# Kernel tuning notes

Measured on AMD Instinct MI355X. Metric: run time of the kernel, lower is better.

Reference implementation:

```python
import jax, jax.numpy as jnp
import numpy as np

NUM_HEADS = 32
NUM_KV_HEADS = 8
HEAD_DIM = 128
EPS = 1e-6
ROPE_THETA = 10000.0


def setup_inputs() -> dict:
    key = jax.random.key(0)
    k1, k2, k3 = jax.random.split(key, 3)
    B, S, H = 2, 2048, 4096
    qkv_out = (NUM_HEADS + 2 * NUM_KV_HEADS) * HEAD_DIM  # 6144
    return {
        "hidden_states": jax.random.normal(k1, (B, S, H), dtype=jnp.float32),
        "positions": jnp.arange(S, dtype=jnp.int32),
        "wqkv": jax.random.normal(k2, (qkv_out, H), dtype=jnp.float32) * 0.02,
        "q_norm_w": jnp.ones((HEAD_DIM,), dtype=jnp.float32),
        "k_norm_w": jnp.ones((HEAD_DIM,), dtype=jnp.float32),
        "wo": jax.random.normal(k3, (H, H), dtype=jnp.float32) * 0.02,
    }


def _rmsnorm(x, w, eps=EPS):
    # per-head RMSNorm over last dim (head_dim), computed in fp32
    xf = x.astype(jnp.float32)
    var = jnp.mean(xf * xf, axis=-1, keepdims=True)
    return (xf * jax.lax.rsqrt(var + eps) * w).astype(x.dtype)


def _rope(x, positions):
    # NeoX-style half rotation, rotary_dim == head_dim
    d = x.shape[-1]
    half = d // 2
    inv_freq = 1.0 / (ROPE_THETA ** (jnp.arange(0, half, dtype=jnp.float32) * 2.0 / d))
    ang = positions.astype(jnp.float32)[:, None] * inv_freq[None, :]  # [S, half]
    cos = jnp.cos(ang)[None, :, None, :]  # [1,S,1,half]
    sin = jnp.sin(ang)[None, :, None, :]
    x1, x2 = x[..., :half], x[..., half:]
    return jnp.concatenate([x1 * cos - x2 * sin, x2 * cos + x1 * sin], axis=-1)


def reference(hidden_states, positions, wqkv, q_norm_w, k_norm_w, wo):
    B, S, H = hidden_states.shape
    scale = HEAD_DIM ** -0.5
    qkv = jnp.einsum("bsh,oh->bso", hidden_states, wqkv)
    q_size = NUM_HEADS * HEAD_DIM
    kv_size = NUM_KV_HEADS * HEAD_DIM
    q = qkv[..., :q_size].reshape(B, S, NUM_HEADS, HEAD_DIM)
    k = qkv[..., q_size:q_size + kv_size].reshape(B, S, NUM_KV_HEADS, HEAD_DIM)
    v = qkv[..., q_size + kv_size:].reshape(B, S, NUM_KV_HEADS, HEAD_DIM)
    q = _rmsnorm(q, q_norm_w)
    k = _rmsnorm(k, k_norm_w)
    q = _rope(q, positions)
    k = _rope(k, positions)
    # GQA: expand kv heads to query heads
    group = NUM_HEADS // NUM_KV_HEADS
    k = jnp.repeat(k, group, axis=2)  # [B,S,NUM_HEADS,D]
    v = jnp.repeat(v, group, axis=2)
    scores = jnp.einsum("bqhd,bkhd->bhqk", q, k) * scale
    causal = jnp.tril(jnp.ones((S, S), dtype=bool))
    scores = jnp.where(causal[None, None], scores, jnp.finfo(scores.dtype).min)
    probs = jax.nn.softmax(scores, axis=-1)
    attn = jnp.einsum("bhqk,bkhd->bqhd", probs, v).reshape(B, S, NUM_HEADS * HEAD_DIM)
    return jnp.einsum("bsi,oi->bso", attn, wo)
```

## Files before the change

### kernel.cpp

```cpp
#include <hip/hip_runtime.h>
#include <hip/hip_bf16.h>
#include <cstdint>
#include <cstddef>

typedef __hip_bfloat16 bf16;
typedef __attribute__((ext_vector_type(8))) short s8v;
typedef __attribute__((ext_vector_type(4))) float f4v;

#define NH 32
#define NKV 8
#define HD 128
#define BB 2
#define SS 2048
#define HH 4096
#define QKVO 6144
#define MM 4096

__device__ __forceinline__ void gld_lds16(const void* g, void* l) {
    __builtin_amdgcn_global_load_lds(
        (const __attribute__((address_space(1))) void*)g,
        (__attribute__((address_space(3))) void*)l, 16, 0, 0);
}

#define MFMA_BF16(a, b, c) __builtin_amdgcn_mfma_f32_16x16x32_bf16((a), (b), (c), 0, 0, 0)

struct alignas(16) bf16x8s { bf16 v[8]; };
__global__ __launch_bounds__(256) void conv_kernel(const float* __restrict__ in,
                                                   bf16* __restrict__ out, int n8) {
    int i = blockIdx.x * 256 + threadIdx.x;
    if (i >= n8) return;
    const float4* in4 = (const float4*)in;
    float4 a = in4[i * 2];
    float4 b = in4[i * 2 + 1];
    bf16x8s p;
    p.v[0] = __float2bfloat16(a.x); p.v[1] = __float2bfloat16(a.y);
    p.v[2] = __float2bfloat16(a.z); p.v[3] = __float2bfloat16(a.w);
    p.v[4] = __float2bfloat16(b.x); p.v[5] = __float2bfloat16(b.y);
    p.v[6] = __float2bfloat16(b.z); p.v[7] = __float2bfloat16(b.w);
    *(bf16x8s*)(out + (size_t)i * 8) = p;
}

__device__ __forceinline__ void stage_half(const bf16* __restrict__ gbase, int ldg,
                                           int kt, int h, bf16* lbase, int tid) {
    int srow = tid >> 3;
    int slot = (tid & 7) ^ (srow & 7);
    const bf16* g = gbase + (size_t)(h * 128 + srow) * ldg + (size_t)kt * 64 + slot * 8;
    char* l = (char*)lbase + h * 16384 + tid * 16;
    gld_lds16(g, l);
    gld_lds16(g + (size_t)64 * ldg, l + 8192);
}

template <typename OutT>
__global__ __launch_bounds__(512, 2) void gemm_bt256(const bf16* __restrict__ A,
                                                     const bf16* __restrict__ Bm,
                                                     OutT* __restrict__ C,
                                                     int M, int N, int K) {
    __shared__ bf16 sA[2][256 * 64];
    __shared__ bf16 sB[2][256 * 64];
    const int tid = threadIdx.x;
    const int lane = tid & 63;
    const int wave = tid >> 6;
    const int l15 = lane & 15, quad = lane >> 4;
    const int wm = wave >> 2;
    const int wn = wave & 3;

    const int nbn = N >> 8;
    const int nwg = (M >> 8) * nbn;
    const int orig = blockIdx.y * gridDim.x + blockIdx.x;
    const int cpx = nwg >> 3;
    const int swz = (orig & 7) * cpx + (orig >> 3);
    const int bm = swz / nbn, bn = swz % nbn;

    const bf16* Ab = A + (size_t)bm * 256 * K;
    const bf16* Bb = Bm + (size_t)bn * 256 * K;
    const int NT = K >> 6;

    const int soff0 = (quad ^ (l15 & 7)) << 4;
    const int ra  = (wm * 128 + l15) * 128;
    const int rbb = (wn * 64 + l15) * 128;
#define LDA(p, m, k) (*(const s8v*)((const char*)sA[p] + ra  + (m) * 2048 + (soff0 ^ ((k) << 6))))
#define LDB(p, n, k) (*(const s8v*)((const char*)sB[p] + rbb + (n) * 2048 + (soff0 ^ ((k) << 6))))

    f4v acc[8][4] = {};
    s8v a[4][2], b0[2][2], b1[2][2];

    stage_half(Bb, K, 0, 0, sB[0], tid);
    stage_half(Ab, K, 0, 0, sA[0], tid);
    stage_half(Bb, K, 0, 1, sB[0], tid);
    stage_half(Ab, K, 0, 1, sA[0], tid);
    stage_half(Bb, K, 1, 0, sB[1], tid);
    stage_half(Ab, K, 1, 0, sA[1], tid);
    asm volatile("s_waitcnt vmcnt(4)" ::: "memory");
    __builtin_amdgcn_s_barrier();

    for (int t = 0; t < NT; ++t) {
        const int p = t & 1;
#pragma unroll
        for (int m = 0; m < 4; ++m) { a[m][0] = LDA(p, m, 0); a[m][1] = LDA(p, m, 1); }
#pragma unroll
        for (int n = 0; n < 2; ++n) { b0[n][0] = LDB(p, n, 0); b0[n][1] = LDB(p, n, 1); }
        if (t + 1 < NT) stage_half(Bb, K, t + 1, 1, sB[p ^ 1], tid);
        asm volatile("s_waitcnt lgkmcnt(8)" ::: "memory");
        __builtin_amdgcn_s_barrier();
        asm volatile("s_waitcnt lgkmcnt(0)" ::: "memory");
        __builtin_amdgcn_sched_barrier(0);
        __builtin_amdgcn_s_setprio(1);
#pragma unroll
        for (int m = 0; m < 4; ++m)
#pragma unroll
            for (int n = 0; n < 2; ++n) {
                acc[m][n] = MFMA_BF16(a[m][0], b0[n][0], acc[m][n]);
                acc[m][n] = MFMA_BF16(a[m][1], b0[n][1], acc[m][n]);
            }
        __builtin_amdgcn_s_setprio(0);
        __builtin_amdgcn_s_barrier();
#pragma unroll
        for (int n = 0; n < 2; ++n) { b1[n][0] = LDB(p, n + 2, 0); b1[n][1] = LDB(p, n + 2, 1); }
        if (t + 1 < NT) stage_half(Ab, K, t + 1, 1, sA[p ^ 1], tid);
        __builtin_amdgcn_s_barrier();
        asm volatile("s_waitcnt lgkmcnt(0)" ::: "memory");
        __builtin_amdgcn_sched_barrier(0);
        __builtin_amdgcn_s_setprio(1);
#pragma unroll
        for (int m = 0; m < 4; ++m)
#pragma unroll
            for (int n = 0; n < 2; ++n) {
                acc[m][n + 2] = MFMA_BF16(a[m][0], b1[n][0], acc[m][n + 2]);
                acc[m][n + 2] = MFMA_BF16(a[m][1], b1[n][1], acc[m][n + 2]);
            }
        __builtin_amdgcn_s_setprio(0);
        __builtin_amdgcn_s_barrier();
#pragma unroll
        for (int m = 0; m < 4; ++m) { a[m][0] = LDA(p, m + 4, 0); a[m][1] = LDA(p, m + 4, 1); }
        if (t + 2 < NT) stage_half(Bb, K, t + 2, 0, sB[p], tid);
        __builtin_amdgcn_s_barrier();
        asm volatile("s_waitcnt lgkmcnt(0)" ::: "memory");
        __builtin_amdgcn_sched_barrier(0);
        __builtin_amdgcn_s_setprio(1);
#pragma unroll
        for (int m = 0; m < 4; ++m)
#pragma unroll
            for (int n = 0; n < 2; ++n) {
                acc[m + 4][n + 2] = MFMA_BF16(a[m][0], b1[n][0], acc[m + 4][n + 2]);
                acc[m + 4][n + 2] = MFMA_BF16(a[m][1], b1[n][1], acc[m + 4][n + 2]);
            }
        __builtin_amdgcn_s_setprio(0);
        __builtin_amdgcn_s_barrier();
        if (t + 2 < NT) stage_half(Ab, K, t + 2, 0, sA[p], tid);
        __builtin_amdgcn_s_barrier();
        __builtin_amdgcn_s_setprio(1);
#pragma unroll
        for (int m = 0; m < 4; ++m)
#pragma unroll
            for (int n = 0; n < 2; ++n) {
                acc[m + 4][n] = MFMA_BF16(a[m][0], b0[n][0], acc[m + 4][n]);
                acc[m + 4][n] = MFMA_BF16(a[m][1], b0[n][1], acc[m + 4][n]);
            }
        __builtin_amdgcn_s_setprio(0);
        if (t + 2 < NT) { asm volatile("s_waitcnt vmcnt(4)" ::: "memory"); }
        else            { asm volatile("s_waitcnt vmcnt(0)" ::: "memory"); }
        __builtin_amdgcn_s_barrier();
    }
#undef LDA
#undef LDB

#pragma unroll
    for (int m = 0; m < 8; ++m)
#pragma unroll
        for (int n = 0; n < 4; ++n) {
            int r0 = bm * 256 + wm * 128 + m * 16 + quad * 4;
            int c0 = bn * 256 + wn * 64 + n * 16 + l15;
#pragma unroll
            for (int r = 0; r < 4; ++r) {
                float v = acc[m][n][r];
                if constexpr (sizeof(OutT) == 2)
                    C[(size_t)(r0 + r) * N + c0] = (OutT)__float2bfloat16(v);
                else
                    C[(size_t)(r0 + r) * N + c0] = (OutT)v;
            }
        }
}

__global__ __launch_bounds__(128) void norm_rope_kernel(
    const bf16* __restrict__ qkv, const int* __restrict__ positions,
    const float* __restrict__ qw, const float* __restrict__ kw,
    bf16* __restrict__ qb, bf16* __restrict__ kb) {
    int rowid = blockIdx.x;
    int head = blockIdx.y;
    int d = threadIdx.x;
    int b = rowid >> 11, s = rowid & 2047;
    bool isq = head < NH;
    int col = isq ? head * HD + d : NH * HD + (head - NH) * HD + d;
    float x = __bfloat162float(qkv[(size_t)rowid * QKVO + col]);

    __shared__ float sv[128];
    __shared__ float partial[2];
    float ss = x * x;
#pragma unroll
    for (int off = 32; off; off >>= 1) ss += __shfl_xor(ss, off, 64);
    if ((threadIdx.x & 63) == 0) partial[threadIdx.x >> 6] = ss;
    __syncthreads();
    float var = (partial[0] + partial[1]) * (1.0f / 128.0f);
    float w = isq ? qw[d] : kw[d];
    float xn = x * rsqrtf(var + 1e-6f) * w;
    sv[d] = xn;
    __syncthreads();

    float pos = (float)positions[s];
    float o;
    if (d < 64) {
        float ang = pos * exp2f(-(float)d * 0.20762051f);
        float c, si; __sincosf(ang, &si, &c);
        o = xn * c - sv[d + 64] * si;
    } else {
        int i = d - 64;
        float ang = pos * exp2f(-(float)i * 0.20762051f);
        float c, si; __sincosf(ang, &si, &c);
        o = xn * c + sv[i] * si;
    }
    if (isq) o *= 0.08838834764831845f;
    size_t oidx;
    if (isq) oidx = (((size_t)(b * NH + head) * SS + s) * HD + d);
    else     oidx = (((size_t)(b * NKV + (head - NH)) * SS + s) * HD + d);
    (isq ? qb : kb)[oidx] = __float2bfloat16(o);
}

__global__ __launch_bounds__(256) void vtrans_kernel(const bf16* __restrict__ qkv,
                                                     bf16* __restrict__ vt) {
    int bh = blockIdx.z;
    int s0 = blockIdx.x * 32, d0 = blockIdx.y * 32;
    int b = bh >> 3, hv = bh & 7;
    __shared__ bf16 tile[32][33];
    int tx = threadIdx.x, ty = threadIdx.y;
    size_t colbase = (size_t)(NH + NKV) * HD + hv * HD + d0;
    for (int i = 0; i < 4; i++) {
        int s = s0 + ty + i * 8;
        tile[ty + i * 8][tx] = qkv[(size_t)(b * SS + s) * QKVO + colbase + tx];
    }
    __syncthreads();
    for (int i = 0; i < 4; i++) {
        int d = d0 + ty + i * 8;
        vt[((size_t)(bh * HD + d)) * SS + s0 + tx] = tile[tx][ty + i * 8];
    }
}

__global__ __launch_bounds__(512, 4) void attn_kernel(
    const bf16* __restrict__ q, const bf16* __restrict__ k,
    const bf16* __restrict__ vt, bf16* __restrict__ out) {
    int pi = blockIdx.x;
    int h = blockIdx.y;
    int b = blockIdx.z;
    int hk = h >> 2;
    int tid = threadIdx.x, lane = tid & 63, wave = tid >> 6;
    int l15 = lane & 15, quad = lane >> 4;

    __shared__ bf16 sK[64][136];
    __shared__ bf16 sVt[128][72];
    __shared__ bf16 sP[8][16][72];

    const bf16* qg = q + ((size_t)(b * NH + h) * SS) * HD;
    const bf16* kg = k + ((size_t)(b * NKV + hk) * SS) * HD;
    const bf16* vg = vt + ((size_t)(b * NKV + hk) * HD) * SS;

    for (int half = 0; half < 2; half++) {
        int qt = half ? (15 - pi) : pi;
        int q0 = qt * 128;
        int qrow = q0 + wave * 16 + l15;
        s8v qf[4];
#pragma unroll
        for (int kc = 0; kc < 4; kc++)
            qf[kc] = *(const s8v*)(qg + (size_t)qrow * HD + kc * 32 + quad * 8);

        f4v o[8] = {};
        float lp[4] = {0.f, 0.f, 0.f, 0.f};
        int qgrow[4];
#pragma unroll
        for (int r = 0; r < 4; r++) qgrow[r] = q0 + wave * 16 + quad * 4 + r;

        int nkt = 2 * qt + 2;
        for (int kt = 0; kt < nkt; kt++) {
            int kbase = kt * 64;
            __syncthreads();
#pragma unroll
            for (int it = 0; it < 2; it++) {
                int c = tid + it * 512;
                int r = c >> 4, c8 = (c & 15) * 8;
                *(float4*)(&sK[r][c8]) =
                    *(const float4*)(kg + (size_t)(kbase + r) * HD + c8);
            }
#pragma unroll
            for (int it = 0; it < 2; it++) {
                int c = tid + it * 512;
                int dr = c >> 3, ck = (c & 7) * 8;
                *(float4*)(&sVt[dr][ck]) =
                    *(const float4*)(vg + (size_t)dr * SS + kbase + ck);
            }
            __syncthreads();

            f4v sc[4];
#pragma unroll
            for (int nt = 0; nt < 4; nt++) {
                f4v a = {0.f, 0.f, 0.f, 0.f};
#pragma unroll
                for (int kc = 0; kc < 4; kc++) {
                    s8v bfrag = *(const s8v*)(&sK[nt * 16 + l15][kc * 32 + quad * 8]);
                    a = __builtin_amdgcn_mfma_f32_16x16x32_bf16(qf[kc], bfrag, a, 0, 0, 0);
                }
                sc[nt] = a;
            }
#pragma unroll
            for (int nt = 0; nt < 4; nt++) {
                int kcol = kbase + nt * 16 + l15;
#pragma unroll
                for (int r = 0; r < 4; r++) {
                    float pv = (kcol > qgrow[r]) ? 0.f : __expf(sc[nt][r]);
                    sc[nt][r] = pv;
                    lp[r] += pv;
                }
            }
#pragma unroll
            for (int nt = 0; nt < 4; nt++)
#pragma unroll
                for (int r = 0; r < 4; r++)
                    sP[wave][quad * 4 + r][nt * 16 + l15] = __float2bfloat16(sc[nt][r]);
            asm volatile("s_waitcnt lgkmcnt(0)" ::: "memory");
            s8v pa[2];
#pragma unroll
            for (int kc = 0; kc < 2; kc++)
                pa[kc] = *(const s8v*)(&sP[wave][l15][kc * 32 + quad * 8]);
#pragma unroll
            for (int dt = 0; dt < 8; dt++)
#pragma unroll
                for (int kc = 0; kc < 2; kc++) {
                    s8v vb = *(const s8v*)(&sVt[dt * 16 + l15][kc * 32 + quad * 8]);
                    o[dt] = __builtin_amdgcn_mfma_f32_16x16x32_bf16(pa[kc], vb, o[dt], 0, 0, 0);
                }
        }
#pragma unroll
        for (int off = 1; off < 16; off <<= 1)
#pragma unroll
            for (int r = 0; r < 4; r++) lp[r] += __shfl_xor(lp[r], off, 64);
#pragma unroll
        for (int r = 0; r < 4; r++) {
            float inv = 1.0f / lp[r];
            int sg = qgrow[r];
#pragma unroll
            for (int dt = 0; dt < 8; dt++) {
                int d = dt * 16 + l15;
                out[(((size_t)(b * SS + sg)) * NH + h) * HD + d] =
                    __float2bfloat16(o[dt][r] * inv);
            }
        }
    }
}

extern "C" void kernel_launch(void* const* d_in, const int* in_sizes, int n_in,
                              void* d_out, int out_size, void* d_ws, size_t ws_size,
                              hipStream_t stream) {
    const float* hidden = (const float*)d_in[0];
    const int* positions = (const int*)d_in[1];
    const float* wqkv = (const float*)d_in[2];
    const float* qnw = (const float*)d_in[3];
    const float* knw = (const float*)d_in[4];
    const float* wo = (const float*)d_in[5];
    float* out = (float*)d_out;

    char* ws = (char*)d_ws;
    bf16* hid_bf = (bf16*)ws;
    bf16* wbuf   = (bf16*)(ws + 33554432);
    bf16* qkv    = (bf16*)(ws + 33554432 + 50331648);
    bf16* qb     = (bf16*)(ws + 33554432 + 50331648 + 50331648);
    bf16* kb     = (bf16*)(ws + 33554432 + 50331648 + 50331648 + 33554432);
    bf16* vtb    = (bf16*)(ws + 33554432 + 50331648 + 50331648 + 33554432 + 8388608);
    bf16* attn   = qkv;

    conv_kernel<<<2097152 / 256, 256, 0, stream>>>(hidden, hid_bf, 2097152);
    conv_kernel<<<3145728 / 256, 256, 0, stream>>>(wqkv, wbuf, 3145728);
    gemm_bt256<bf16><<<dim3(16, 24), 512, 0, stream>>>(hid_bf, wbuf, qkv, MM, QKVO, HH);
    norm_rope_kernel<<<dim3(4096, 40), 128, 0, stream>>>(qkv, positions, qnw, knw, qb, kb);
    vtrans_kernel<<<dim3(64, 4, 16), dim3(32, 8), 0, stream>>>(qkv, vtb);
    attn_kernel<<<dim3(8, 32, 2), 512, 0, stream>>>(qb, kb, vtb, attn);
    conv_kernel<<<2097152 / 256, 256, 0, stream>>>(wo, wbuf, 2097152);
    gemm_bt256<float><<<dim3(16, 16), 512, 0, stream>>>(attn, wbuf, out, MM, HH, HH);
}
```

Before: 779.2 us.

## Restructure GEMM global-to-LDS staging into per-wave 8-row loads with deeper prefetch

```diff
diff --git a/kernel.cpp b/kernel.cpp
--- a/kernel.cpp
+++ b/kernel.cpp
@@ -40,14 +40,12 @@
     *(bf16x8s*)(out + (size_t)i * 8) = p;
 }
 
-__device__ __forceinline__ void stage_half(const bf16* __restrict__ gbase, int ldg,
-                                           int kt, int h, bf16* lbase, int tid) {
-    int srow = tid >> 3;
-    int slot = (tid & 7) ^ (srow & 7);
-    const bf16* g = gbase + (size_t)(h * 128 + srow) * ldg + (size_t)kt * 64 + slot * 8;
-    char* l = (char*)lbase + h * 16384 + tid * 16;
-    gld_lds16(g, l);
-    gld_lds16(g + (size_t)64 * ldg, l + 8192);
+__device__ __forceinline__ void stage8(const bf16* __restrict__ g, int ldg, int kt,
+                                       int r0, bf16* lbase, int lane) {
+    int row = r0 + (lane >> 3);
+    int slot = (lane & 7) ^ ((lane >> 3) & 7);
+    gld_lds16(g + (size_t)row * ldg + kt * 64 + slot * 8,
+              (char*)lbase + r0 * 128 + lane * 16);
 }
 
 template <typename OutT>
@@ -75,6 +73,9 @@
     const bf16* Bb = Bm + (size_t)bn * 256 * K;
     const int NT = K >> 6;
 
+    const int aq0 = wave * 8;
+    const int bs0 = (wave >> 2) * 64 + (wave & 3) * 8;
+
     const int soff0 = (quad ^ (l15 & 7)) << 4;
     const int ra  = (wm * 128 + l15) * 128;
     const int rbb = (wn * 64 + l15) * 128;
@@ -84,22 +85,28 @@
     f4v acc[8][4] = {};
     s8v a[4][2], b0[2][2], b1[2][2];
 
-    stage_half(Bb, K, 0, 0, sB[0], tid);
-    stage_half(Ab, K, 0, 0, sA[0], tid);
-    stage_half(Bb, K, 0, 1, sB[0], tid);
-    stage_half(Ab, K, 0, 1, sA[0], tid);
-    stage_half(Bb, K, 1, 0, sB[1], tid);
-    stage_half(Ab, K, 1, 0, sA[1], tid);
-    asm volatile("s_waitcnt vmcnt(4)" ::: "memory");
+#pragma unroll
+    for (int u = 0; u < 2; ++u) {
+        stage8(Ab, K, u, aq0,        sA[u], lane);
+        stage8(Ab, K, u, aq0 + 128,  sA[u], lane);
+        stage8(Bb, K, u, bs0,        sB[u], lane);
+        stage8(Bb, K, u, bs0 + 128,  sB[u], lane);
+        stage8(Bb, K, u, bs0 + 32,   sB[u], lane);
+        stage8(Bb, K, u, bs0 + 160,  sB[u], lane);
+        stage8(Ab, K, u, aq0 + 64,   sA[u], lane);
+        stage8(Ab, K, u, aq0 + 192,  sA[u], lane);
+    }
+    asm volatile("s_waitcnt vmcnt(12)" ::: "memory");
     __builtin_amdgcn_s_barrier();
 
     for (int t = 0; t < NT; ++t) {
         const int p = t & 1;
+        const int kt2 = t + 2;
+        const bool s2 = kt2 < NT;
 #pragma unroll
         for (int m = 0; m < 4; ++m) { a[m][0] = LDA(p, m, 0); a[m][1] = LDA(p, m, 1); }
 #pragma unroll
         for (int n = 0; n < 2; ++n) { b0[n][0] = LDB(p, n, 0); b0[n][1] = LDB(p, n, 1); }
-        if (t + 1 < NT) stage_half(Bb, K, t + 1, 1, sB[p ^ 1], tid);
         asm volatile("s_waitcnt lgkmcnt(8)" ::: "memory");
         __builtin_amdgcn_s_barrier();
         asm volatile("s_waitcnt lgkmcnt(0)" ::: "memory");
@@ -113,10 +120,17 @@
                 acc[m][n] = MFMA_BF16(a[m][1], b0[n][1], acc[m][n]);
             }
         __builtin_amdgcn_s_setprio(0);
+        if (t + 1 < NT) { asm volatile("s_waitcnt vmcnt(10)" ::: "memory"); }
+        else            { asm volatile("s_waitcnt vmcnt(2)"  ::: "memory"); }
         __builtin_amdgcn_s_barrier();
 #pragma unroll
         for (int n = 0; n < 2; ++n) { b1[n][0] = LDB(p, n + 2, 0); b1[n][1] = LDB(p, n + 2, 1); }
-        if (t + 1 < NT) stage_half(Ab, K, t + 1, 1, sA[p ^ 1], tid);
+        if (s2) {
+            stage8(Ab, K, kt2, aq0,       sA[p], lane);
+            stage8(Ab, K, kt2, aq0 + 128, sA[p], lane);
+            stage8(Bb, K, kt2, bs0,       sB[p], lane);
+            stage8(Bb, K, kt2, bs0 + 128, sB[p], lane);
+        }
         __builtin_amdgcn_s_barrier();
         asm volatile("s_waitcnt lgkmcnt(0)" ::: "memory");
         __builtin_amdgcn_sched_barrier(0);
@@ -129,10 +143,16 @@
                 acc[m][n + 2] = MFMA_BF16(a[m][1], b1[n][1], acc[m][n + 2]);
             }
         __builtin_amdgcn_s_setprio(0);
+        if (s2)             { asm volatile("s_waitcnt vmcnt(12)" ::: "memory"); }
+        else if (t + 1 < NT){ asm volatile("s_waitcnt vmcnt(8)"  ::: "memory"); }
+        else                { asm volatile("s_waitcnt vmcnt(0)"  ::: "memory"); }
         __builtin_amdgcn_s_barrier();
 #pragma unroll
         for (int m = 0; m < 4; ++m) { a[m][0] = LDA(p, m + 4, 0); a[m][1] = LDA(p, m + 4, 1); }
-        if (t + 2 < NT) stage_half(Bb, K, t + 2, 0, sB[p], tid);
+        if (s2) {
+            stage8(Bb, K, kt2, bs0 + 32,  sB[p], lane);
+            stage8(Bb, K, kt2, bs0 + 160, sB[p], lane);
+        }
         __builtin_amdgcn_s_barrier();
         asm volatile("s_waitcnt lgkmcnt(0)" ::: "memory");
         __builtin_amdgcn_sched_barrier(0);
@@ -146,8 +166,10 @@
             }
         __builtin_amdgcn_s_setprio(0);
         __builtin_amdgcn_s_barrier();
-        if (t + 2 < NT) stage_half(Ab, K, t + 2, 0, sA[p], tid);
-        __builtin_amdgcn_s_barrier();
+        if (s2) {
+            stage8(Ab, K, kt2, aq0 + 64,  sA[p], lane);
+            stage8(Ab, K, kt2, aq0 + 192, sA[p], lane);
+        }
         __builtin_amdgcn_s_setprio(1);
 #pragma unroll
         for (int m = 0; m < 4; ++m)
@@ -157,8 +179,8 @@
                 acc[m + 4][n] = MFMA_BF16(a[m][1], b0[n][1], acc[m + 4][n]);
             }
         __builtin_amdgcn_s_setprio(0);
-        if (t + 2 < NT) { asm volatile("s_waitcnt vmcnt(4)" ::: "memory"); }
-        else            { asm volatile("s_waitcnt vmcnt(0)" ::: "memory"); }
+        if (s2)              { asm volatile("s_waitcnt vmcnt(12)" ::: "memory"); }
+        else if (t + 1 < NT) { asm volatile("s_waitcnt vmcnt(4)"  ::: "memory"); }
         __builtin_amdgcn_s_barrier();
     }
 #undef LDA
```

After: 791.6 us. No clear change (+1.6%).
